# Kernel optimization log

Measured on AMD Instinct MI355X. Metric: run time of the kernel, lower is better.

## Reference

```python
import jax, jax.numpy as jnp
import numpy as np

N_NODES = 100000


def gcn_conv(x, W, b, edge_index, num_nodes):
    """PyG-style GCNConv: h = D^-1/2 (A + I) D^-1/2 (x W) + b."""
    src, dst = edge_index[0], edge_index[1]
    loop = jnp.arange(num_nodes, dtype=src.dtype)
    src = jnp.concatenate([src, loop])
    dst = jnp.concatenate([dst, loop])
    # degree over A + I (counted on destination, matching PyG gcn_norm)
    deg = jax.ops.segment_sum(jnp.ones_like(dst, dtype=x.dtype), dst, num_segments=num_nodes)
    dinv = jnp.where(deg > 0, jax.lax.rsqrt(deg), 0.0)
    norm = dinv[src] * dinv[dst]  # [E+N]
    h = x @ W  # [N, out]
    msg = h[src] * norm[:, None]  # [E+N, out]
    out = jax.ops.segment_sum(msg, dst, num_segments=num_nodes)
    return out + b


def setup_inputs() -> dict:
    key = jax.random.key(0)
    ks = jax.random.split(key, 13)
    N, D_IN, D_OUT, E = N_NODES, 64, 64, 1250000
    x = jax.random.normal(ks[0], (N, D_IN), dtype=jnp.float32)
    edge_index = jax.random.randint(ks[1], (2, E), 0, N, dtype=jnp.int64)
    edge_index1 = jax.random.randint(ks[2], (2, E), 0, N, dtype=jnp.int64)
    edge_index2 = jax.random.randint(ks[3], (2, E), 0, N, dtype=jnp.int64)
    s = 1.0 / np.sqrt(D_IN)
    W_ln = jax.random.uniform(ks[4], (D_IN, D_OUT), jnp.float32, -s, s)
    b_ln = jax.random.uniform(ks[5], (D_OUT,), jnp.float32, -s, s)
    W1 = jax.random.uniform(ks[6], (D_IN, D_OUT), jnp.float32, -s, s)
    b1 = jnp.zeros((D_OUT,), jnp.float32)
    W2 = jax.random.uniform(ks[7], (D_IN, D_OUT), jnp.float32, -s, s)
    b2 = jnp.zeros((D_OUT,), jnp.float32)
    W3 = jax.random.uniform(ks[8], (D_IN, D_OUT), jnp.float32, -s, s)
    b3 = jnp.zeros((D_OUT,), jnp.float32)
    return {"x": x, "edge_index": edge_index, "edge_index1": edge_index1,
            "edge_index2": edge_index2, "W_ln": W_ln, "b_ln": b_ln,
            "W1": W1, "b1": b1, "W2": W2, "b2": b2, "W3": W3, "b3": b3}


def reference(x, edge_index, edge_index1, edge_index2, W_ln, b_ln, W1, b1, W2, b2, W3, b3):
    N = x.shape[0]
    x0 = x @ W_ln + b_ln
    x1 = gcn_conv(x, W1, b1, edge_index, N)
    x2 = gcn_conv(x, W2, b2, edge_index1, N)
    x3 = gcn_conv(x, W3, b3, edge_index2, N)
    return (x0, x1, x2, x3)
```

## Files before the change

### kernel.cpp

```cpp
#include <hip/hip_runtime.h>
#include <hip/hip_bf16.h>

#define NBKT_MAX 512
#define BIN_CHUNK 8192
#define CSR_CAP 8192

__device__ __forceinline__ unsigned short f2bf(float f) {
    __hip_bfloat16 h = __float2bfloat16(f);
    union { __hip_bfloat16 h; unsigned short u; } cv; cv.h = h; return cv.u;
}
__device__ __forceinline__ float bf2f(unsigned short u) {
    unsigned int b = ((unsigned int)u) << 16;
    union { unsigned int u; float f; } cv; cv.u = b; return cv.f;
}
__device__ __forceinline__ const int* pick(const int* e0, const int* e1, const int* e2, int y) {
    return y == 0 ? e0 : (y == 1 ? e1 : e2);
}

__global__ __launch_bounds__(256) void k_hist(const int* __restrict__ e0, const int* __restrict__ e1,
                                              const int* __restrict__ e2, int E, int nbkt,
                                              int* __restrict__ bucket_cnt) {
    const int* ep = pick(e0, e1, e2, blockIdx.y);
    __shared__ int h[NBKT_MAX];
    for (int i = threadIdx.x; i < NBKT_MAX; i += 256) h[i] = 0;
    __syncthreads();
    int base = blockIdx.x * 4096;
    #pragma unroll
    for (int k = 0; k < 16; k++) {
        int i = base + k * 256 + threadIdx.x;
        if (i < E) atomicAdd(&h[ep[E + i] >> 8], 1);
    }
    __syncthreads();
    for (int i = threadIdx.x; i < nbkt; i += 256)
        if (h[i]) atomicAdd(&bucket_cnt[blockIdx.y * nbkt + i], h[i]);
}

__global__ __launch_bounds__(512) void k_scanb(const int* __restrict__ bucket_cnt,
                                               int* __restrict__ bucket_base,
                                               int* __restrict__ bucket_cursor, int nbkt) {
    __shared__ int s[512];
    int t = threadIdx.x;
    int v = (t < nbkt) ? bucket_cnt[blockIdx.y * nbkt + t] : 0;
    s[t] = v; __syncthreads();
    for (int off = 1; off < 512; off <<= 1) {
        int a = (t >= off) ? s[t - off] : 0;
        __syncthreads();
        s[t] += a;
        __syncthreads();
    }
    if (t < nbkt) {
        int e = s[t] - v;
        bucket_base[blockIdx.y * nbkt + t] = e;
        bucket_cursor[blockIdx.y * nbkt + t] = e;
    }
}

__global__ __launch_bounds__(256) void k_bin(const int* __restrict__ e0, const int* __restrict__ e1,
                                             const int* __restrict__ e2, int E, int nbkt,
                                             int* __restrict__ bucket_cursor,
                                             unsigned int* __restrict__ binned) {
    const int* ep = pick(e0, e1, e2, blockIdx.y);
    __shared__ int h[NBKT_MAX];
    __shared__ int lbase[NBKT_MAX];
    __shared__ int gbase[NBKT_MAX];
    __shared__ unsigned int stg[BIN_CHUNK];
    int t = threadIdx.x;
    h[t] = 0; h[t + 256] = 0;
    __syncthreads();
    int cbase = blockIdx.x * BIN_CHUNK;
    #pragma unroll
    for (int k = 0; k < BIN_CHUNK / 256; k++) {
        int i = cbase + k * 256 + t;
        if (i < E) atomicAdd(&h[ep[E + i] >> 8], 1);
    }
    __syncthreads();
    lbase[t] = h[t]; lbase[t + 256] = h[t + 256];
    __syncthreads();
    for (int off = 1; off < 512; off <<= 1) {
        int a0 = (t >= off) ? lbase[t - off] : 0;
        int i1 = t + 256;
        int a1 = (i1 >= off) ? lbase[i1 - off] : 0;
        __syncthreads();
        lbase[t] += a0; lbase[i1] += a1;
        __syncthreads();
    }
    int c0 = h[t], c1 = h[t + 256];
    int ex0 = lbase[t] - c0, ex1 = lbase[t + 256] - c1;
    if (t < nbkt && c0) gbase[t] = atomicAdd(&bucket_cursor[blockIdx.y * nbkt + t], c0);
    int i1g = t + 256;
    if (i1g < nbkt && c1) gbase[i1g] = atomicAdd(&bucket_cursor[blockIdx.y * nbkt + i1g], c1);
    __syncthreads();
    lbase[t] = ex0; lbase[t + 256] = ex1;
    h[t] = 0; h[t + 256] = 0;
    __syncthreads();
    #pragma unroll
    for (int k = 0; k < BIN_CHUNK / 256; k++) {
        int i = cbase + k * 256 + t;
        if (i < E) {
            int s = ep[i];
            int d = ep[E + i];
            int b = d >> 8;
            int lp = atomicAdd(&h[b], 1);
            stg[lbase[b] + lp] = ((unsigned)s << 8) | (unsigned)(d & 255);
        }
    }
    __syncthreads();
    unsigned int* bout = binned + (size_t)blockIdx.y * E;
    int sg = t >> 4, lane = t & 15;
    for (int b = sg; b < nbkt; b += 16) {
        int n = h[b];
        if (!n) continue;
        int lb = lbase[b];
        unsigned int* dst = bout + gbase[b];
        for (int i = lane; i < n; i += 16) dst[i] = stg[lb + i];
    }
}

__global__ __launch_bounds__(256) void k_csr(const unsigned int* __restrict__ binned,
                                             const int* __restrict__ bucket_cnt,
                                             const int* __restrict__ bucket_base,
                                             int E, int N, int nbkt,
                                             int* __restrict__ cnt, int* __restrict__ row_start,
                                             int* __restrict__ sorted) {
    int b = blockIdx.x, conv = blockIdx.y, t = threadIdx.x;
    __shared__ int c[256];
    __shared__ int sc[256];
    __shared__ unsigned int stg[CSR_CAP];
    int segbase = bucket_base[conv * nbkt + b];
    int segcnt  = bucket_cnt[conv * nbkt + b];
    const unsigned int* bin = binned + (size_t)conv * E + segbase;

    c[t] = 0; __syncthreads();
    for (int i = t; i < segcnt; i += 256) atomicAdd(&c[bin[i] & 255], 1);
    __syncthreads();

    int v = c[t];
    sc[t] = v; __syncthreads();
    for (int off = 1; off < 256; off <<= 1) {
        int a = (t >= off) ? sc[t - off] : 0;
        __syncthreads();
        sc[t] += a;
        __syncthreads();
    }
    int ex = sc[t] - v;
    int node = (b << 8) + t;
    if (node < N) {
        cnt[conv * N + node] = v;
        row_start[conv * N + node] = segbase + ex;
    }
    __syncthreads();
    c[t] = ex;
    __syncthreads();
    int* so = sorted + (size_t)conv * E + segbase;
    if (segcnt <= CSR_CAP) {
        for (int i = t; i < segcnt; i += 256) {
            unsigned p = bin[i];
            int pos = atomicAdd(&c[p & 255], 1);
            stg[pos] = p >> 8;
        }
        __syncthreads();
        for (int i = t; i < segcnt; i += 256) so[i] = (int)stg[i];
    } else {
        for (int i = t; i < segcnt; i += 256) {
            unsigned p = bin[i];
            int pos = atomicAdd(&c[p & 255], 1);
            so[pos] = (int)(p >> 8);
        }
    }
}

#define GSTEP(XK, KC)                                                              \
    do {                                                                           \
        const float xk_ = (XK);                                                    \
        float4 w_;                                                                 \
        w_ = *(const float4*)(Wbase + 0 * 4096 + (KC) * 64);                       \
        a0.x += xk_ * w_.x; a0.y += xk_ * w_.y; a0.z += xk_ * w_.z; a0.w += xk_ * w_.w; \
        w_ = *(const float4*)(Wbase + 1 * 4096 + (KC) * 64);                       \
        a1.x += xk_ * w_.x; a1.y += xk_ * w_.y; a1.z += xk_ * w_.z; a1.w += xk_ * w_.w; \
        w_ = *(const float4*)(Wbase + 2 * 4096 + (KC) * 64);                       \
        a2.x += xk_ * w_.x; a2.y += xk_ * w_.y; a2.z += xk_ * w_.z; a2.w += xk_ * w_.w; \
        w_ = *(const float4*)(Wbase + 3 * 4096 + (KC) * 64);                       \
        a3.x += xk_ * w_.x; a3.y += xk_ * w_.y; a3.z += xk_ * w_.z; a3.w += xk_ * w_.w; \
    } while (0)

__global__ __launch_bounds__(256) void k_gemm(
    const float* __restrict__ x,
    const float* __restrict__ Wln, const float* __restrict__ bln,
    const float* __restrict__ W1, const float* __restrict__ W2,
    const float* __restrict__ W3,
    const int* __restrict__ cnt, int N,
    float* __restrict__ out0, unsigned short* __restrict__ g) {
    __shared__ float Wl[4 * 4096];
    int t = threadIdx.x;
    const float* Ws[4] = {Wln, W1, W2, W3};
    #pragma unroll
    for (int m = 0; m < 4; m++)
        for (int i = t; i < 4096; i += 256) Wl[m * 4096 + i] = Ws[m][i];
    __syncthreads();

    int r = blockIdx.x * 256 + t;
    if (r >= N) return;

    float4 xv[16];
    const float4* xr = (const float4*)(x + (size_t)r * 64);
    #pragma unroll
    for (int i = 0; i < 16; i++) xv[i] = xr[i];

    float dinv0 = rsqrtf((float)(cnt[0 * N + r] + 1));
    float dinv1 = rsqrtf((float)(cnt[1 * N + r] + 1));
    float dinv2 = rsqrtf((float)(cnt[2 * N + r] + 1));

    const size_t NB = (size_t)N * 64;
    float* orow = out0 + (size_t)r * 64;
    unsigned short* g0 = g + 0 * NB + (size_t)r * 64;
    unsigned short* g1 = g + 1 * NB + (size_t)r * 64;
    unsigned short* g2 = g + 2 * NB + (size_t)r * 64;

    for (int j4 = 0; j4 < 16; j4++) {
        float4 a0 = make_float4(0.f, 0.f, 0.f, 0.f), a1 = a0, a2 = a0, a3 = a0;
        const float* Wbase = Wl + j4 * 4;
        #pragma unroll
        for (int k4 = 0; k4 < 16; k4++) {
            const float4 xk4 = xv[k4];
            GSTEP(xk4.x, k4 * 4 + 0);
            GSTEP(xk4.y, k4 * 4 + 1);
            GSTEP(xk4.z, k4 * 4 + 2);
            GSTEP(xk4.w, k4 * 4 + 3);
        }
        float4 bl = ((const float4*)bln)[j4];
        float4 o = make_float4(a0.x + bl.x, a0.y + bl.y, a0.z + bl.z, a0.w + bl.w);
        ((float4*)orow)[j4] = o;
        ushort4 u;
        u.x = f2bf(a1.x * dinv0); u.y = f2bf(a1.y * dinv0);
        u.z = f2bf(a1.z * dinv0); u.w = f2bf(a1.w * dinv0);
        ((ushort4*)g0)[j4] = u;
        u.x = f2bf(a2.x * dinv1); u.y = f2bf(a2.y * dinv1);
        u.z = f2bf(a2.z * dinv1); u.w = f2bf(a2.w * dinv1);
        ((ushort4*)g1)[j4] = u;
        u.x = f2bf(a3.x * dinv2); u.y = f2bf(a3.y * dinv2);
        u.z = f2bf(a3.z * dinv2); u.w = f2bf(a3.w * dinv2);
        ((ushort4*)g2)[j4] = u;
    }
}

__global__ __launch_bounds__(256) void k_gather(
    const unsigned short* __restrict__ g, const int* __restrict__ sorted,
    const int* __restrict__ row_start, const int* __restrict__ cnt,
    const float* __restrict__ b1, const float* __restrict__ b2,
    const float* __restrict__ b3,
    int N, int E, float* __restrict__ out) {
    int t = threadIdx.x;
    int node = blockIdx.x * 16 + (t >> 4);
    int l = t & 15;
    int conv = blockIdx.y;
    if (node >= N) return;

    const size_t NB = (size_t)N * 64;
    const unsigned short* gm = g + (size_t)conv * NB;
    int rs = row_start[conv * N + node];
    int ne = cnt[conv * N + node];
    const int* sp = sorted + (size_t)conv * E + rs;

    ushort4 su = ((const ushort4*)(gm + (size_t)node * 64))[l];
    float4 acc = make_float4(bf2f(su.x), bf2f(su.y), bf2f(su.z), bf2f(su.w));

    int j = 0;
    for (; j + 4 <= ne; j += 4) {
        int s0 = sp[j], s1 = sp[j + 1], s2 = sp[j + 2], s3 = sp[j + 3];
        ushort4 u0 = ((const ushort4*)(gm + (size_t)s0 * 64))[l];
        ushort4 u1 = ((const ushort4*)(gm + (size_t)s1 * 64))[l];
        ushort4 u2 = ((const ushort4*)(gm + (size_t)s2 * 64))[l];
        ushort4 u3 = ((const ushort4*)(gm + (size_t)s3 * 64))[l];
        acc.x += bf2f(u0.x) + bf2f(u1.x) + bf2f(u2.x) + bf2f(u3.x);
        acc.y += bf2f(u0.y) + bf2f(u1.y) + bf2f(u2.y) + bf2f(u3.y);
        acc.z += bf2f(u0.z) + bf2f(u1.z) + bf2f(u2.z) + bf2f(u3.z);
        acc.w += bf2f(u0.w) + bf2f(u1.w) + bf2f(u2.w) + bf2f(u3.w);
    }
    for (; j < ne; j++) {
        int s = sp[j];
        ushort4 u = ((const ushort4*)(gm + (size_t)s * 64))[l];
        acc.x += bf2f(u.x); acc.y += bf2f(u.y);
        acc.z += bf2f(u.z); acc.w += bf2f(u.w);
    }

    float dv = rsqrtf((float)(ne + 1));
    const float* bp = conv == 0 ? b1 : (conv == 1 ? b2 : b3);
    float4 bb = ((const float4*)bp)[l];
    float4 o = make_float4(acc.x * dv + bb.x, acc.y * dv + bb.y,
                           acc.z * dv + bb.z, acc.w * dv + bb.w);
    ((float4*)(out + (size_t)(1 + conv) * NB + (size_t)node * 64))[l] = o;
}

extern "C" void kernel_launch(void* const* d_in, const int* in_sizes, int n_in,
                              void* d_out, int out_size, void* d_ws, size_t ws_size,
                              hipStream_t stream) {
    const float* x   = (const float*)d_in[0];
    const int*   e0  = (const int*)d_in[1];
    const int*   e1  = (const int*)d_in[2];
    const int*   e2  = (const int*)d_in[3];
    const float* Wln = (const float*)d_in[4];
    const float* bln = (const float*)d_in[5];
    const float* W1  = (const float*)d_in[6];
    const float* b1  = (const float*)d_in[7];
    const float* W2  = (const float*)d_in[8];
    const float* b2  = (const float*)d_in[9];
    const float* W3  = (const float*)d_in[10];
    const float* b3  = (const float*)d_in[11];

    int N = in_sizes[0] / 64;
    int E = in_sizes[1] / 2;
    int nbkt = (N + 255) >> 8;
    float* out = (float*)d_out;

    char* w = (char*)d_ws;
    auto alloc = [&](size_t bytes) {
        char* p = w;
        w += (bytes + 255) / 256 * 256;
        return p;
    };
    unsigned short* g      = (unsigned short*)alloc((size_t)3 * N * 64 * 2);
    int* cnt               = (int*)alloc((size_t)3 * N * 4);
    int* row_start         = (int*)alloc((size_t)3 * N * 4);
    int* sorted            = (int*)alloc((size_t)3 * E * 4);
    unsigned int* binned   = (unsigned int*)alloc((size_t)3 * E * 4);
    int* bucket_cnt        = (int*)alloc((size_t)3 * nbkt * 4);
    int* bucket_base       = (int*)alloc((size_t)3 * nbkt * 4);
    int* bucket_cursor     = (int*)alloc((size_t)3 * nbkt * 4);

    hipMemsetAsync(bucket_cnt, 0, (size_t)3 * nbkt * 4, stream);

    k_hist<<<dim3((E + 4095) / 4096, 3), 256, 0, stream>>>(e0, e1, e2, E, nbkt, bucket_cnt);
    k_scanb<<<dim3(1, 3), 512, 0, stream>>>(bucket_cnt, bucket_base, bucket_cursor, nbkt);
    k_bin<<<dim3((E + BIN_CHUNK - 1) / BIN_CHUNK, 3), 256, 0, stream>>>(e0, e1, e2, E, nbkt,
                                                                        bucket_cursor, binned);
    k_csr<<<dim3(nbkt, 3), 256, 0, stream>>>(binned, bucket_cnt, bucket_base, E, N, nbkt,
                                             cnt, row_start, sorted);
    k_gemm<<<dim3((N + 255) / 256), 256, 0, stream>>>(x, Wln, bln, W1, W2, W3,
                                                      cnt, N, out, g);
    k_gather<<<dim3((N + 15) / 16, 3), 256, 0, stream>>>(g, sorted, row_start, cnt,
                                                         b1, b2, b3, N, E, out);
}
```

Measured before the change: 411.3 us.

## Restructure dense GEMM to register-resident weight columns with shared-memory x tiles

```diff
diff --git a/kernel.cpp b/kernel.cpp
--- a/kernel.cpp
+++ b/kernel.cpp
@@ -4,6 +4,7 @@
 #define NBKT_MAX 512
 #define BIN_CHUNK 8192
 #define CSR_CAP 8192
+#define GR 256
 
 __device__ __forceinline__ unsigned short f2bf(float f) {
     __hip_bfloat16 h = __float2bfloat16(f);
@@ -169,77 +170,66 @@
     }
 }
 
-#define GSTEP(XK, KC)                                                              \
-    do {                                                                           \
-        const float xk_ = (XK);                                                    \
-        float4 w_;                                                                 \
-        w_ = *(const float4*)(Wbase + 0 * 4096 + (KC) * 64);                       \
-        a0.x += xk_ * w_.x; a0.y += xk_ * w_.y; a0.z += xk_ * w_.z; a0.w += xk_ * w_.w; \
-        w_ = *(const float4*)(Wbase + 1 * 4096 + (KC) * 64);                       \
-        a1.x += xk_ * w_.x; a1.y += xk_ * w_.y; a1.z += xk_ * w_.z; a1.w += xk_ * w_.w; \
-        w_ = *(const float4*)(Wbase + 2 * 4096 + (KC) * 64);                       \
-        a2.x += xk_ * w_.x; a2.y += xk_ * w_.y; a2.z += xk_ * w_.z; a2.w += xk_ * w_.w; \
-        w_ = *(const float4*)(Wbase + 3 * 4096 + (KC) * 64);                       \
-        a3.x += xk_ * w_.x; a3.y += xk_ * w_.y; a3.z += xk_ * w_.z; a3.w += xk_ * w_.w; \
-    } while (0)
-
-__global__ __launch_bounds__(256) void k_gemm(
+__global__ __launch_bounds__(512) void k_gemm(
     const float* __restrict__ x,
     const float* __restrict__ Wln, const float* __restrict__ bln,
     const float* __restrict__ W1, const float* __restrict__ W2,
     const float* __restrict__ W3,
     const int* __restrict__ cnt, int N,
     float* __restrict__ out0, unsigned short* __restrict__ g) {
-    __shared__ float Wl[4 * 4096];
+    __shared__ float xs[GR * 64];
     int t = threadIdx.x;
-    const float* Ws[4] = {Wln, W1, W2, W3};
+    int base = blockIdx.x * GR;
+    int rows = min(GR, N - base);
+
+    {
+        int nv = rows * 16;
+        const float4* xg = (const float4*)(x + (size_t)base * 64);
+        float4* xsv = (float4*)xs;
+        for (int i = t; i < nv; i += 512) xsv[i] = xg[i];
+    }
+
+    int w = t >> 6;
+    int lane = t & 63;
+    int pair = w & 1;
+    int wi = w >> 1;
+
+    const float* WA = pair == 0 ? Wln : W2;
+    const float* WB = pair == 0 ? W1 : W3;
+    float wa[64], wb[64];
     #pragma unroll
-    for (int m = 0; m < 4; m++)
-        for (int i = t; i < 4096; i += 256) Wl[m * 4096 + i] = Ws[m][i];
-    __syncthreads();
-
-    int r = blockIdx.x * 256 + t;
-    if (r >= N) return;
-
-    float4 xv[16];
-    const float4* xr = (const float4*)(x + (size_t)r * 64);
-    #pragma unroll
-    for (int i = 0; i < 16; i++) xv[i] = xr[i];
-
-    float dinv0 = rsqrtf((float)(cnt[0 * N + r] + 1));
-    float dinv1 = rsqrtf((float)(cnt[1 * N + r] + 1));
-    float dinv2 = rsqrtf((float)(cnt[2 * N + r] + 1));
+    for (int k = 0; k < 64; k++) {
+        wa[k] = WA[k * 64 + lane];
+        wb[k] = WB[k * 64 + lane];
+    }
+    float bl = (pair == 0) ? bln[lane] : 0.f;
+    __syncthreads();
 
     const size_t NB = (size_t)N * 64;
-    float* orow = out0 + (size_t)r * 64;
-    unsigned short* g0 = g + 0 * NB + (size_t)r * 64;
-    unsigned short* g1 = g + 1 * NB + (size_t)r * 64;
-    unsigned short* g2 = g + 2 * NB + (size_t)r * 64;
-
-    for (int j4 = 0; j4 < 16; j4++) {
-        float4 a0 = make_float4(0.f, 0.f, 0.f, 0.f), a1 = a0, a2 = a0, a3 = a0;
-        const float* Wbase = Wl + j4 * 4;
+    int r0 = wi * (GR / 4);
+    int r1 = min(r0 + GR / 4, rows);
+    for (int r = r0; r < r1; r++) {
+        const float4* xr = (const float4*)(xs + r * 64);
+        float accA = 0.f, accB = 0.f;
         #pragma unroll
         for (int k4 = 0; k4 < 16; k4++) {
-            const float4 xk4 = xv[k4];
-            GSTEP(xk4.x, k4 * 4 + 0);
-            GSTEP(xk4.y, k4 * 4 + 1);
-            GSTEP(xk4.z, k4 * 4 + 2);
-            GSTEP(xk4.w, k4 * 4 + 3);
-        }
-        float4 bl = ((const float4*)bln)[j4];
-        float4 o = make_float4(a0.x + bl.x, a0.y + bl.y, a0.z + bl.z, a0.w + bl.w);
-        ((float4*)orow)[j4] = o;
-        ushort4 u;
-        u.x = f2bf(a1.x * dinv0); u.y = f2bf(a1.y * dinv0);
-        u.z = f2bf(a1.z * dinv0); u.w = f2bf(a1.w * dinv0);
-        ((ushort4*)g0)[j4] = u;
-        u.x = f2bf(a2.x * dinv1); u.y = f2bf(a2.y * dinv1);
-        u.z = f2bf(a2.z * dinv1); u.w = f2bf(a2.w * dinv1);
-        ((ushort4*)g1)[j4] = u;
-        u.x = f2bf(a3.x * dinv2); u.y = f2bf(a3.y * dinv2);
-        u.z = f2bf(a3.z * dinv2); u.w = f2bf(a3.w * dinv2);
-        ((ushort4*)g2)[j4] = u;
+            float4 xv = xr[k4];
+            accA += xv.x * wa[k4 * 4 + 0]; accB += xv.x * wb[k4 * 4 + 0];
+            accA += xv.y * wa[k4 * 4 + 1]; accB += xv.y * wb[k4 * 4 + 1];
+            accA += xv.z * wa[k4 * 4 + 2]; accB += xv.z * wb[k4 * 4 + 2];
+            accA += xv.w * wa[k4 * 4 + 3]; accB += xv.w * wb[k4 * 4 + 3];
+        }
+        int gr = base + r;
+        if (pair == 0) {
+            out0[(size_t)gr * 64 + lane] = accA + bl;
+            float d0 = rsqrtf((float)(cnt[gr] + 1));
+            g[(size_t)gr * 64 + lane] = f2bf(accB * d0);
+        } else {
+            float d1 = rsqrtf((float)(cnt[N + gr] + 1));
+            float d2 = rsqrtf((float)(cnt[2 * N + gr] + 1));
+            g[NB + (size_t)gr * 64 + lane] = f2bf(accA * d1);
+            g[2 * NB + (size_t)gr * 64 + lane] = f2bf(accB * d2);
+        }
     }
 }
 
@@ -335,8 +325,8 @@
                                                                         bucket_cursor, binned);
     k_csr<<<dim3(nbkt, 3), 256, 0, stream>>>(binned, bucket_cnt, bucket_base, E, N, nbkt,
                                              cnt, row_start, sorted);
-    k_gemm<<<dim3((N + 255) / 256), 256, 0, stream>>>(x, Wln, bln, W1, W2, W3,
-                                                      cnt, N, out, g);
+    k_gemm<<<dim3((N + GR - 1) / GR), 512, 0, stream>>>(x, Wln, bln, W1, W2, W3,
+                                                        cnt, N, out, g);
     k_gather<<<dim3((N + 15) / 16, 3), 256, 0, stream>>>(g, sorted, row_start, cnt,
                                                          b1, b2, b3, N, E, out);
 }
```

Result: faster. 396.1 us (-3.7%).
